# Kernel optimization log

Measured on AMD Instinct MI355X. Metric: run time of the kernel, lower is better.

## Reference

```python
import jax, jax.numpy as jnp
import numpy as np

N, C, IN_DIM, H_DIM, NUM_DEP = 16384, 4, 300, 512, 48


def setup_inputs() -> dict:
    key = jax.random.key(0)
    ks = jax.random.split(key, 12)
    # --- tree structure: 4-ary heap, reversed so children have SMALLER index than parent; root = N-1 ---
    i = np.arange(N)
    j = (N - 1) - i                                   # heap index (root j=0)
    cj = C * j[:, None] + 1 + np.arange(C)[None, :]   # heap indices of children [N,C]
    valid = cj <= N - 1
    child_idx = np.where(valid, (N - 1) - cj, 0).astype(np.int32)
    mask_h = valid.astype(np.float32)
    mask_e = valid.astype(np.float32)
    rng = np.random.default_rng(0)
    child_dep = rng.integers(0, NUM_DEP, size=(N, C)).astype(np.int32)
    leaf = ~valid.any(axis=1)
    # torch leaf branch: one virtual child with h=zeros and dep index 0
    mask_e[leaf, 0] = 1.0
    child_dep[leaf, 0] = 0
    child_idx[leaf, 0] = 0
    s = 0.02  # weight scale (stands in for xavier init)
    lin = lambda k, o, d: (jax.random.normal(k, (o, d), jnp.float32) * s)
    return {
        "x": jax.random.normal(ks[0], (N, IN_DIM), jnp.float32),
        "child_idx": jnp.asarray(child_idx),
        "child_dep": jnp.asarray(child_dep),
        "mask_h": jnp.asarray(mask_h),
        "mask_e": jnp.asarray(mask_e),
        "demb": jax.random.normal(ks[1], (NUM_DEP, H_DIM), jnp.float32) * s,
        "iux_w": lin(ks[2], 2 * H_DIM, IN_DIM), "iux_b": jnp.zeros((2 * H_DIM,), jnp.float32),
        "iuh_w": lin(ks[3], 2 * H_DIM, H_DIM), "iuh_b": jnp.zeros((2 * H_DIM,), jnp.float32),
        "iue_w": lin(ks[4], 2 * H_DIM, H_DIM), "iue_b": jnp.zeros((2 * H_DIM,), jnp.float32),
        "fx_w": lin(ks[5], H_DIM, IN_DIM), "fx_b": jnp.zeros((H_DIM,), jnp.float32),
        "fh_w": lin(ks[6], H_DIM, H_DIM), "fh_b": jnp.zeros((H_DIM,), jnp.float32),
        "fe_w": lin(ks[7], H_DIM, H_DIM), "fe_b": jnp.zeros((H_DIM,), jnp.float32),
    }


def reference(x, child_idx, child_dep, mask_h, mask_e, demb,
              iux_w, iux_b, iuh_w, iuh_b, iue_w, iue_b,
              fx_w, fx_b, fh_w, fh_b, fe_w, fe_b):
    n, h_dim = x.shape[0], fh_w.shape[0]

    def step(H, xs):
        t, xt, cidx, cdep, mh, me = xs
        ch = H[cidx] * mh[:, None]            # [C,h] child hiddens (zeros for pad / leaf virtual child)
        e = demb[cdep]                        # [C,h] dependency embeddings
        h_sum = ch.sum(0)                     # child-sum h
        e_sum = (e * me[:, None]).sum(0)      # child-sum dep embedding (leaf -> demb[0])
        iu = (xt @ iux_w.T + iux_b) + (h_sum @ iuh_w.T + iuh_b) + (e_sum @ iue_w.T + iue_b)
        i_g = jax.nn.sigmoid(iu[:h_dim])
        u = jnp.tanh(iu[h_dim:])
        f = jax.nn.sigmoid(ch @ fh_w.T + fh_b + (xt @ fx_w.T + fx_b) + e @ fe_w.T + fe_b)  # [C,h]
        h_new = jnp.tanh(i_g * u + (f * ch).sum(0))   # padded rows contribute 0 since ch=0
        return H.at[t].set(h_new), None

    H0 = jnp.zeros((n, h_dim), x.dtype)
    xs = (jnp.arange(n), x, child_idx, child_dep, mask_h, mask_e)
    Hf, _ = jax.lax.scan(step, H0, xs)
    return Hf[n - 1][None, :]   # root hidden state, shape [1, h_dim]
```

## Files before the change

kernel.cpp:

```cpp
#include <hip/hip_runtime.h>
#include <cstddef>

#define N_NODES 16384
#define HD      512
#define INDIM   300
#define INP     320
#define NDEP    48
#define NLEAF   10923
#define KT      32
#define LM      16
#define LCOL    128

typedef unsigned int u32;
typedef unsigned short u16;
typedef __attribute__((ext_vector_type(8))) short short8;
typedef __attribute__((ext_vector_type(4))) float f32x4;

typedef __attribute__((address_space(1))) const u32 as1_u32;
typedef __attribute__((address_space(3))) u32 as3_u32;

__device__ __forceinline__ float sigmoidf_(float v) {
    return 1.f / (1.f + __expf(-v));
}
__device__ __forceinline__ float tanhf_(float v) {
    v = fminf(15.f, fmaxf(-15.f, v));
    const float e = __expf(2.f * v);
    return (e - 1.f) / (e + 1.f);
}
__device__ __forceinline__ u16 f2bf(float f) {
    u32 u = __float_as_uint(f);
    u32 r = (u + 0x7fffu + ((u >> 16) & 1u)) >> 16;
    return (u16)r;
}
__device__ __forceinline__ float b2f(u16 v) {
    return __uint_as_float((u32)v << 16);
}
__device__ __forceinline__ u32 pack2(float a, float b) {
    return (u32)f2bf(a) | ((u32)f2bf(b) << 16);
}

__global__ __launch_bounds__(256)
void emb_proj_kernel(const float* __restrict__ demb,
                     const float* __restrict__ iue_w,
                     const float* __restrict__ fe_w,
                     const float* __restrict__ iux_b,
                     const float* __restrict__ iuh_b,
                     const float* __restrict__ iue_b,
                     const float* __restrict__ fx_b,
                     const float* __restrict__ fh_b,
                     const float* __restrict__ fe_b,
                     float* __restrict__ iemb,
                     float* __restrict__ femb,
                     float* __restrict__ ibc,
                     float* __restrict__ fbc)
{
    const int bo  = blockIdx.x;
    const int tid = threadIdx.x;
    if (bo == 384) {
        for (int o = tid; o < 1024; o += 256) ibc[o] = iux_b[o] + iuh_b[o] + iue_b[o];
        for (int o = tid; o < 512;  o += 256) fbc[o] = fx_b[o] + fh_b[o] + fe_b[o];
        return;
    }
    const int wave = tid >> 6;
    const int d    = tid & 63;
    const bool isI = (bo < 256);
    const int o    = (isI ? bo : bo - 256) * 4 + wave;
    const float* wrow = isI ? (iue_w + (size_t)o * HD) : (fe_w + (size_t)o * HD);
    if (d >= NDEP) return;
    const float* drow = demb + (size_t)d * HD;

    float4 a0 = make_float4(0.f, 0.f, 0.f, 0.f);
    float4 a1 = make_float4(0.f, 0.f, 0.f, 0.f);
    for (int k = 0; k < HD; k += 8) {
        const float4 wv0 = *reinterpret_cast<const float4*>(wrow + k);
        const float4 wv1 = *reinterpret_cast<const float4*>(wrow + k + 4);
        const float4 dv0 = *reinterpret_cast<const float4*>(drow + k);
        const float4 dv1 = *reinterpret_cast<const float4*>(drow + k + 4);
        a0.x = fmaf(dv0.x, wv0.x, a0.x); a0.y = fmaf(dv0.y, wv0.y, a0.y);
        a0.z = fmaf(dv0.z, wv0.z, a0.z); a0.w = fmaf(dv0.w, wv0.w, a0.w);
        a1.x = fmaf(dv1.x, wv1.x, a1.x); a1.y = fmaf(dv1.y, wv1.y, a1.y);
        a1.z = fmaf(dv1.z, wv1.z, a1.z); a1.w = fmaf(dv1.w, wv1.w, a1.w);
    }
    const float s = ((a0.x + a0.y) + (a0.z + a0.w)) + ((a1.x + a1.y) + (a1.z + a1.w));
    if (isI) iemb[(size_t)d * 1024 + o] = s;
    else     femb[(size_t)d * 512  + o] = s;
}

#define CV_T0 (N_NODES * INP)
#define CV_T1 (1536 * INP)
#define CV_T2 (1536 * HD)

__global__ __launch_bounds__(256)
void convert_all_kernel(const float* __restrict__ x,
                        const float* __restrict__ iux_w, const float* __restrict__ fx_w,
                        const float* __restrict__ iuh_w, const float* __restrict__ fh_w,
                        u16* __restrict__ xb, u16* __restrict__ WXb, u16* __restrict__ WHb)
{
    const int idx = blockIdx.x * 256 + threadIdx.x;
    if (idx < CV_T0) {
        const int r = idx / INP, k = idx - r * INP;
        xb[idx] = f2bf(k < INDIM ? x[(size_t)r * INDIM + k] : 0.f);
    } else if (idx < CV_T0 + CV_T1) {
        const int i2 = idx - CV_T0;
        const int r = i2 / INP, k = i2 - r * INP;
        float v = 0.f;
        if (k < INDIM) v = (r < 1024) ? iux_w[(size_t)r * INDIM + k]
                                      : fx_w[(size_t)(r - 1024) * INDIM + k];
        WXb[i2] = f2bf(v);
    } else {
        const int i3 = idx - CV_T0 - CV_T1;
        const int r = i3 >> 9, k = i3 & 511;
        const float v = (r < 1024) ? iuh_w[(size_t)r * HD + k]
                                   : fh_w[(size_t)(r - 1024) * HD + k];
        WHb[i3] = f2bf(v);
    }
}

__device__ __forceinline__
void gemm_body(u16* As, u16* Bs,
               const u16* __restrict__ A, int lda,
               const u16* __restrict__ B, int ldb,
               u16* __restrict__ C, int ldc,
               int M, int K, int bx, int by)
{
    const int tid  = threadIdx.x;
    const int lane = tid & 63;
    const int wave = tid >> 6;
    const int mBlk = bx * 128;
    const int nBlk = by * 128;

    const int wr = (wave >> 1) * 64;
    const int wc = (wave & 1) * 64;
    const int fr = lane & 15;
    const int kg = lane >> 4;

    f32x4 acc[4][4];
    #pragma unroll
    for (int i = 0; i < 4; ++i)
        #pragma unroll
        for (int j = 0; j < 4; ++j) acc[i][j] = (f32x4){0.f, 0.f, 0.f, 0.f};

    int offA[4], offB[4];
    #pragma unroll
    for (int it = 0; it < 4; ++it) {
        const int s   = it * 256 + tid;
        const int row = s >> 3, c = s & 7;
        const int cs  = c ^ (row & 7);
        int ga = mBlk + row; if (ga > M - 1) ga = M - 1;
        offA[it] = ga * lda + cs * 8;
        offB[it] = (nBlk + row) * ldb + cs * 8;
    }

    for (int k0 = 0; k0 < K; k0 += 64) {
        #pragma unroll
        for (int it = 0; it < 4; ++it) {
            const int ldsOff = (it * 256 + wave * 64) * 8;
            __builtin_amdgcn_global_load_lds((as1_u32*)(A + offA[it] + k0),
                                             (as3_u32*)(&As[ldsOff]), 16, 0, 0);
            __builtin_amdgcn_global_load_lds((as1_u32*)(B + offB[it] + k0),
                                             (as3_u32*)(&Bs[ldsOff]), 16, 0, 0);
        }
        __syncthreads();
        #pragma unroll
        for (int half = 0; half < 2; ++half) {
            const int ckb = half * 4 + kg;
            short8 af[4], bf[4];
            #pragma unroll
            for (int f = 0; f < 4; ++f) {
                const int ar = wr + f * 16 + fr;
                af[f] = *(const short8*)&As[ar * 64 + ((ckb ^ (ar & 7)) * 8)];
                const int br = wc + f * 16 + fr;
                bf[f] = *(const short8*)&Bs[br * 64 + ((ckb ^ (br & 7)) * 8)];
            }
            #pragma unroll
            for (int mi = 0; mi < 4; ++mi)
                #pragma unroll
                for (int ni = 0; ni < 4; ++ni)
                    acc[mi][ni] = __builtin_amdgcn_mfma_f32_16x16x32_bf16(
                                      af[mi], bf[ni], acc[mi][ni], 0, 0, 0);
        }
        __syncthreads();
    }

    #pragma unroll
    for (int mi = 0; mi < 4; ++mi) {
        const int r0 = mBlk + wr + mi * 16 + kg * 4;
        #pragma unroll
        for (int v = 0; v < 4; ++v) {
            const int r = r0 + v;
            if (r >= M) continue;
            u16* crow = C + (size_t)r * ldc + nBlk + wc + fr;
            #pragma unroll
            for (int ni = 0; ni < 4; ++ni)
                crow[ni * 16] = f2bf(acc[mi][ni][v]);
        }
    }
}

__global__ __launch_bounds__(256, 2)
void gemm_bf16_dual_kernel(const u16* __restrict__ A1, int lda1,
                           const u16* __restrict__ B1, int ldb1,
                           u16* __restrict__ C1, int ldc1, int M1, int K1,
                           int gx1, int n1,
                           const u16* __restrict__ A2, int lda2,
                           const u16* __restrict__ B2, int ldb2,
                           u16* __restrict__ C2, int ldc2, int M2, int K2,
                           int gx2)
{
    __shared__ u16 As[128 * 64];
    __shared__ u16 Bs[128 * 64];
    const int flat = blockIdx.x;
    if (flat < n1) {
        gemm_body(As, Bs, A1, lda1, B1, ldb1, C1, ldc1, M1, K1,
                  flat % gx1, flat / gx1);
    } else {
        const int f2 = flat - n1;
        gemm_body(As, Bs, A2, lda2, B2, ldb2, C2, ldc2, M2, K2,
                  f2 % gx2, f2 / gx2);
    }
}

__global__ __launch_bounds__(256)
void fused_leaf_kernel(const u16* __restrict__ XPiub,
                       const float* __restrict__ iemb, const float* __restrict__ ibc,
                       const int* __restrict__ cidx, const float* __restrict__ mh,
                       float* __restrict__ H, u16* __restrict__ Hb,
                       u16* __restrict__ HSB, int loNext)
{
    const int g   = blockIdx.x;
    const int p   = loNext + g;
    const int j2  = threadIdx.x * 2;

    int ct[4]; float cm[4];
    #pragma unroll
    for (int c = 0; c < 4; ++c) { ct[c] = cidx[p * 4 + c]; cm[c] = mh[p * 4 + c]; }

    const float2 ibci = *reinterpret_cast<const float2*>(&ibc[j2]);
    const float2 ibcu = *reinterpret_cast<const float2*>(&ibc[512 + j2]);
    const float2 iei  = *reinterpret_cast<const float2*>(&iemb[j2]);
    const float2 ieu  = *reinterpret_cast<const float2*>(&iemb[512 + j2]);

    float hs0 = 0.f, hs1 = 0.f;
    #pragma unroll
    for (int c = 0; c < 4; ++c) {
        if (cm[c] == 0.f) continue;
        const int t = ct[c];
        const u32 xi = *reinterpret_cast<const u32*>(&XPiub[(size_t)t * 1024 + j2]);
        const u32 xu = *reinterpret_cast<const u32*>(&XPiub[(size_t)t * 1024 + 512 + j2]);
        const float h0 = tanhf_(sigmoidf_(b2f((u16)xi) + iei.x + ibci.x)
                                * tanhf_(b2f((u16)xu) + ieu.x + ibcu.x));
        const float h1 = tanhf_(sigmoidf_(b2f((u16)(xi >> 16)) + iei.y + ibci.y)
                                * tanhf_(b2f((u16)(xu >> 16)) + ieu.y + ibcu.y));
        *reinterpret_cast<float2*>(&H[(size_t)t * 512 + j2]) = make_float2(h0, h1);
        *reinterpret_cast<u32*>(&Hb[(size_t)t * 512 + j2]) = pack2(h0, h1);
        hs0 += h0; hs1 += h1;
    }
    *reinterpret_cast<u32*>(&HSB[(size_t)g * 512 + j2]) = pack2(hs0, hs1);
}

__global__ __launch_bounds__(256)
void fused_combine_kernel(const u16* __restrict__ XPiub, const u16* __restrict__ XPfb,
                          const u16* __restrict__ PIUb, const u16* __restrict__ GFb,
                          const int* __restrict__ cidx, const int* __restrict__ cdep,
                          const float* __restrict__ mh, const float* __restrict__ me,
                          const float* __restrict__ iemb, const float* __restrict__ femb,
                          const float* __restrict__ ibc, const float* __restrict__ fbc,
                          float* __restrict__ H, u16* __restrict__ Hb,
                          u16* __restrict__ HSB,
                          int lo, int loNext, int isRoot, float* __restrict__ outp)
{
    const int j2 = threadIdx.x * 2;

    int ct[4]; float cm[4];
    if (isRoot) {
        ct[0] = N_NODES - 1; cm[0] = 1.f;
        ct[1] = ct[2] = ct[3] = 0; cm[1] = cm[2] = cm[3] = 0.f;
    } else {
        const int p = loNext + blockIdx.x;
        #pragma unroll
        for (int c = 0; c < 4; ++c) { ct[c] = cidx[p * 4 + c]; cm[c] = mh[p * 4 + c]; }
    }

    const float2 ibci = *reinterpret_cast<const float2*>(&ibc[j2]);
    const float2 ibcu = *reinterpret_cast<const float2*>(&ibc[512 + j2]);
    const float2 fbc2 = *reinterpret_cast<const float2*>(&fbc[j2]);

    float hs0 = 0.f, hs1 = 0.f;
    #pragma unroll
    for (int c = 0; c < 4; ++c) {
        if (cm[c] == 0.f) continue;
        const int t = ct[c];

        int ci2[4], dp2[4]; float m2[4], e2[4];
        #pragma unroll
        for (int k = 0; k < 4; ++k) {
            ci2[k] = cidx[t * 4 + k]; dp2[k] = cdep[t * 4 + k];
            m2[k]  = mh[t * 4 + k];   e2[k]  = me[t * 4 + k];
        }

        float ei0 = 0.f, ei1 = 0.f, eu0 = 0.f, eu1 = 0.f;
        #pragma unroll
        for (int k = 0; k < 4; ++k) {
            if (e2[k] != 0.f) {
                const float* ie = iemb + (size_t)dp2[k] * 1024;
                const float2 a = *reinterpret_cast<const float2*>(&ie[j2]);
                const float2 b = *reinterpret_cast<const float2*>(&ie[512 + j2]);
                ei0 = fmaf(e2[k], a.x, ei0); ei1 = fmaf(e2[k], a.y, ei1);
                eu0 = fmaf(e2[k], b.x, eu0); eu1 = fmaf(e2[k], b.y, eu1);
            }
        }

        const u32 xi = *reinterpret_cast<const u32*>(&XPiub[(size_t)t * 1024 + j2]);
        const u32 xu = *reinterpret_cast<const u32*>(&XPiub[(size_t)t * 1024 + 512 + j2]);
        const u32 pi = *reinterpret_cast<const u32*>(&PIUb[(size_t)(t - lo) * 1024 + j2]);
        const u32 pu = *reinterpret_cast<const u32*>(&PIUb[(size_t)(t - lo) * 1024 + 512 + j2]);
        const u32 xf = *reinterpret_cast<const u32*>(&XPfb[(size_t)(t - NLEAF) * 512 + j2]);

        const float iu_i0 = b2f((u16)xi) + b2f((u16)pi) + ibci.x + ei0;
        const float iu_i1 = b2f((u16)(xi >> 16)) + b2f((u16)(pi >> 16)) + ibci.y + ei1;
        const float iu_u0 = b2f((u16)xu) + b2f((u16)pu) + ibcu.x + eu0;
        const float iu_u1 = b2f((u16)(xu >> 16)) + b2f((u16)(pu >> 16)) + ibcu.y + eu1;
        const float xf0 = b2f((u16)xf) + fbc2.x;
        const float xf1 = b2f((u16)(xf >> 16)) + fbc2.y;

        float fcs0 = 0.f, fcs1 = 0.f;
        #pragma unroll
        for (int k = 0; k < 4; ++k) {
            if (m2[k] != 0.f) {
                const u32 gf = *reinterpret_cast<const u32*>(&GFb[(size_t)ci2[k] * 512 + j2]);
                const float2 fe = *reinterpret_cast<const float2*>(&femb[(size_t)dp2[k] * 512 + j2]);
                const float2 hc = *reinterpret_cast<const float2*>(&H[(size_t)ci2[k] * 512 + j2]);
                const float fv0 = b2f((u16)gf) + xf0 + fe.x;
                const float fv1 = b2f((u16)(gf >> 16)) + xf1 + fe.y;
                fcs0 = fmaf(sigmoidf_(fv0), m2[k] * hc.x, fcs0);
                fcs1 = fmaf(sigmoidf_(fv1), m2[k] * hc.y, fcs1);
            }
        }

        const float h0 = tanhf_(fmaf(sigmoidf_(iu_i0), tanhf_(iu_u0), fcs0));
        const float h1 = tanhf_(fmaf(sigmoidf_(iu_i1), tanhf_(iu_u1), fcs1));
        *reinterpret_cast<float2*>(&H[(size_t)t * 512 + j2]) = make_float2(h0, h1);
        *reinterpret_cast<u32*>(&Hb[(size_t)t * 512 + j2]) = pack2(h0, h1);
        hs0 += h0; hs1 += h1;
        if (isRoot) *reinterpret_cast<float2*>(&outp[j2]) = make_float2(h0, h1);
    }
    if (!isRoot)
        *reinterpret_cast<u32*>(&HSB[(size_t)blockIdx.x * 512 + j2]) = pack2(hs0, hs1);
}

__global__ __launch_bounds__(256)
void emb_setup_kernel(const float* __restrict__ demb,
                      const float* __restrict__ iue_w,
                      const float* __restrict__ fe_w,
                      const float* __restrict__ iux_b,
                      const float* __restrict__ iuh_b,
                      const float* __restrict__ iue_b,
                      const float* __restrict__ fx_b,
                      const float* __restrict__ fh_b,
                      const float* __restrict__ fe_b,
                      float* __restrict__ iemb,
                      float* __restrict__ femb,
                      float* __restrict__ ibc,
                      float* __restrict__ fbc)
{
    const int d   = blockIdx.x;
    const int tid = threadIdx.x;
    __shared__ float sd[HD];
    sd[tid]       = demb[d * HD + tid];
    sd[tid + 256] = demb[d * HD + 256 + tid];
    __syncthreads();

    #pragma unroll
    for (int r = 0; r < 4; ++r) {
        const int o = r * 256 + tid;
        const float* w = iue_w + (size_t)o * HD;
        float acc = 0.f;
        for (int k = 0; k < HD; k += 4) {
            const float4 wv = *reinterpret_cast<const float4*>(w + k);
            acc += sd[k] * wv.x + sd[k + 1] * wv.y + sd[k + 2] * wv.z + sd[k + 3] * wv.w;
        }
        iemb[(size_t)d * 1024 + o] = acc;
    }
    #pragma unroll
    for (int r = 0; r < 2; ++r) {
        const int o = r * 256 + tid;
        const float* w = fe_w + (size_t)o * HD;
        float acc = 0.f;
        for (int k = 0; k < HD; k += 4) {
            const float4 wv = *reinterpret_cast<const float4*>(w + k);
            acc += sd[k] * wv.x + sd[k + 1] * wv.y + sd[k + 2] * wv.z + sd[k + 3] * wv.w;
        }
        femb[(size_t)d * HD + o] = acc;
    }
    if (d == 0) {
        #pragma unroll
        for (int r = 0; r < 4; ++r) { const int o = r * 256 + tid; ibc[o] = iux_b[o] + iuh_b[o] + iue_b[o]; }
        #pragma unroll
        for (int r = 0; r < 2; ++r) { const int o = r * 256 + tid; fbc[o] = fx_b[o] + fh_b[o] + fe_b[o]; }
    }
}

__global__ __launch_bounds__(256, 2)
void level_kernel(const float* __restrict__ x,
                  const int*   __restrict__ child_idx,
                  const int*   __restrict__ child_dep,
                  const float* __restrict__ mask_h,
                  const float* __restrict__ mask_e,
                  const float* __restrict__ iux_w,
                  const float* __restrict__ iuh_w,
                  const float* __restrict__ fx_w,
                  const float* __restrict__ fh_w,
                  const float* __restrict__ iemb,
                  const float* __restrict__ femb,
                  const float* __restrict__ ibc,
                  const float* __restrict__ fbc,
                  float* __restrict__ H,
                  int tLo, int tEnd)
{
    __shared__ __align__(16) float sA[KT][68];
    __shared__ float sWI[KT][LCOL + 1];
    __shared__ float sWU[KT][LCOL + 1];
    __shared__ float sWF[KT][LCOL + 1];
    __shared__ int   sCidx[LM][4];
    __shared__ float sMh[LM][4];
    __shared__ int   sDep[LM][4];
    __shared__ float sMe[LM][4];

    const int tid  = threadIdx.x;
    const int base = tLo + blockIdx.x * LM;
    const int j0   = blockIdx.y * LCOL;

    if (tid < LM * 4) {
        const int m = tid >> 2, c = tid & 3;
        const int t = base + m;
        const bool v = (t < tEnd);
        sCidx[m][c] = v ? child_idx[t * 4 + c] : 0;
        sMh[m][c]   = v ? mask_h[t * 4 + c]    : 0.f;
        sDep[m][c]  = v ? child_dep[t * 4 + c] : 0;
        sMe[m][c]   = v ? mask_e[t * 4 + c]    : 0.f;
    }

    const int jj = tid & 63;
    const int mg = tid >> 6;

    float acc_i[4][2], acc_u[4][2], acc_fx[4][2], acc_f[4][2][4];
    #pragma unroll
    for (int mm = 0; mm < 4; ++mm)
        #pragma unroll
        for (int c2 = 0; c2 < 2; ++c2) {
            acc_i[mm][c2] = 0.f; acc_u[mm][c2] = 0.f; acc_fx[mm][c2] = 0.f;
            #pragma unroll
            for (int c = 0; c < 4; ++c) acc_f[mm][c2][c] = 0.f;
        }

    __syncthreads();

    for (int k0 = 0; k0 < HD; k0 += KT) {
        #pragma unroll
        for (int it = 0; it < 2; ++it) {
            const int chunk = tid + it * 256;
            const int mc = chunk >> 3;
            const int kk = (chunk & 7) * 4;
            const int m = mc >> 2, c = mc & 3;
            const float mhv = sMh[m][c];
            float4 v = make_float4(0.f, 0.f, 0.f, 0.f);
            if (mhv != 0.f)
                v = *reinterpret_cast<const float4*>(H + (size_t)sCidx[m][c] * HD + k0 + kk);
            sA[kk + 0][mc] = v.x; sA[kk + 1][mc] = v.y; sA[kk + 2][mc] = v.z; sA[kk + 3][mc] = v.w;
        }
        #pragma unroll
        for (int it = 0; it < 4; ++it) {
            const int chunk = tid + it * 256;
            const int row = chunk >> 3;
            const int kk = (chunk & 7) * 4;
            const float4 vI = *reinterpret_cast<const float4*>(iuh_w + (size_t)(j0 + row) * HD + k0 + kk);
            const float4 vU = *reinterpret_cast<const float4*>(iuh_w + (size_t)(j0 + row + 512) * HD + k0 + kk);
            const float4 vF = *reinterpret_cast<const float4*>(fh_w  + (size_t)(j0 + row) * HD + k0 + kk);
            sWI[kk + 0][row] = vI.x; sWI[kk + 1][row] = vI.y; sWI[kk + 2][row] = vI.z; sWI[kk + 3][row] = vI.w;
            sWU[kk + 0][row] = vU.x; sWU[kk + 1][row] = vU.y; sWU[kk + 2][row] = vU.z; sWU[kk + 3][row] = vU.w;
            sWF[kk + 0][row] = vF.x; sWF[kk + 1][row] = vF.y; sWF[kk + 2][row] = vF.z; sWF[kk + 3][row] = vF.w;
        }
        __syncthreads();
        #pragma unroll 4
        for (int k = 0; k < KT; ++k) {
            const float wi0 = sWI[k][jj], wi1 = sWI[k][jj + 64];
            const float wu0 = sWU[k][jj], wu1 = sWU[k][jj + 64];
            const float wf0 = sWF[k][jj], wf1 = sWF[k][jj + 64];
            #pragma unroll
            for (int mm = 0; mm < 4; ++mm) {
                const int m = mg + mm * 4;
                const float4 cv = *reinterpret_cast<const float4*>(&sA[k][m * 4]);
                const float hs = (cv.x + cv.y) + (cv.z + cv.w);
                acc_i[mm][0] = fmaf(hs, wi0, acc_i[mm][0]);
                acc_i[mm][1] = fmaf(hs, wi1, acc_i[mm][1]);
                acc_u[mm][0] = fmaf(hs, wu0, acc_u[mm][0]);
                acc_u[mm][1] = fmaf(hs, wu1, acc_u[mm][1]);
                acc_f[mm][0][0] = fmaf(cv.x, wf0, acc_f[mm][0][0]);
                acc_f[mm][1][0] = fmaf(cv.x, wf1, acc_f[mm][1][0]);
                acc_f[mm][0][1] = fmaf(cv.y, wf0, acc_f[mm][0][1]);
                acc_f[mm][1][1] = fmaf(cv.y, wf1, acc_f[mm][1][1]);
                acc_f[mm][0][2] = fmaf(cv.z, wf0, acc_f[mm][0][2]);
                acc_f[mm][1][2] = fmaf(cv.z, wf1, acc_f[mm][1][2]);
                acc_f[mm][0][3] = fmaf(cv.w, wf0, acc_f[mm][0][3]);
                acc_f[mm][1][3] = fmaf(cv.w, wf1, acc_f[mm][1][3]);
            }
        }
        __syncthreads();
    }

    for (int k0 = 0; k0 < INDIM; k0 += KT) {
        if (tid < 128) {
            const int m = tid >> 3;
            const int kk = (tid & 7) * 4;
            const int t = base + m;
            float4 v = make_float4(0.f, 0.f, 0.f, 0.f);
            if (t < tEnd && (k0 + kk + 3) < INDIM)
                v = *reinterpret_cast<const float4*>(x + (size_t)t * INDIM + k0 + kk);
            sA[kk + 0][m] = v.x; sA[kk + 1][m] = v.y; sA[kk + 2][m] = v.z; sA[kk + 3][m] = v.w;
        }
        #pragma unroll
        for (int it = 0; it < 4; ++it) {
            const int chunk = tid + it * 256;
            const int row = chunk >> 3;
            const int kk = (chunk & 7) * 4;
            float4 vI = make_float4(0.f, 0.f, 0.f, 0.f), vU = vI, vF = vI;
            if ((k0 + kk + 3) < INDIM) {
                vI = *reinterpret_cast<const float4*>(iux_w + (size_t)(j0 + row) * INDIM + k0 + kk);
                vU = *reinterpret_cast<const float4*>(iux_w + (size_t)(j0 + row + 512) * INDIM + k0 + kk);
                vF = *reinterpret_cast<const float4*>(fx_w  + (size_t)(j0 + row) * INDIM + k0 + kk);
            }
            sWI[kk + 0][row] = vI.x; sWI[kk + 1][row] = vI.y; sWI[kk + 2][row] = vI.z; sWI[kk + 3][row] = vI.w;
            sWU[kk + 0][row] = vU.x; sWU[kk + 1][row] = vU.y; sWU[kk + 2][row] = vU.z; sWU[kk + 3][row] = vU.w;
            sWF[kk + 0][row] = vF.x; sWF[kk + 1][row] = vF.y; sWF[kk + 2][row] = vF.z; sWF[kk + 3][row] = vF.w;
        }
        __syncthreads();
        #pragma unroll 4
        for (int k = 0; k < KT; ++k) {
            const float wi0 = sWI[k][jj], wi1 = sWI[k][jj + 64];
            const float wu0 = sWU[k][jj], wu1 = sWU[k][jj + 64];
            const float wf0 = sWF[k][jj], wf1 = sWF[k][jj + 64];
            #pragma unroll
            for (int mm = 0; mm < 4; ++mm) {
                const float xv = sA[k][mg + mm * 4];
                acc_i[mm][0]  = fmaf(xv, wi0, acc_i[mm][0]);
                acc_i[mm][1]  = fmaf(xv, wi1, acc_i[mm][1]);
                acc_u[mm][0]  = fmaf(xv, wu0, acc_u[mm][0]);
                acc_u[mm][1]  = fmaf(xv, wu1, acc_u[mm][1]);
                acc_fx[mm][0] = fmaf(xv, wf0, acc_fx[mm][0]);
                acc_fx[mm][1] = fmaf(xv, wf1, acc_fx[mm][1]);
            }
        }
        __syncthreads();
    }

    #pragma unroll
    for (int mm = 0; mm < 4; ++mm) {
        const int m = mg + mm * 4;
        const int t = base + m;
        if (t >= tEnd) continue;
        #pragma unroll
        for (int c2 = 0; c2 < 2; ++c2) {
            const int j = j0 + c2 * 64 + jj;
            float emb_i = 0.f, emb_u = 0.f;
            #pragma unroll
            for (int c = 0; c < 4; ++c) {
                const float mev = sMe[m][c];
                if (mev != 0.f) {
                    const float* ie = iemb + (size_t)sDep[m][c] * 1024;
                    emb_i = fmaf(mev, ie[j], emb_i);
                    emb_u = fmaf(mev, ie[j + 512], emb_u);
                }
            }
            const float iu_i = acc_i[mm][c2] + ibc[j] + emb_i;
            const float iu_u = acc_u[mm][c2] + ibc[j + 512] + emb_u;
            const float ig = sigmoidf_(iu_i);
            const float uu = tanhf_(iu_u);
            float fcs = 0.f;
            #pragma unroll
            for (int c = 0; c < 4; ++c) {
                const float mhv = sMh[m][c];
                if (mhv != 0.f) {
                    const float fv = acc_f[mm][c2][c] + acc_fx[mm][c2] + fbc[j]
                                   + femb[(size_t)sDep[m][c] * HD + j];
                    const float fg = sigmoidf_(fv);
                    const float chj = H[(size_t)sCidx[m][c] * HD + j] * mhv;
                    fcs = fmaf(fg, chj, fcs);
                }
            }
            H[(size_t)t * HD + j] = tanhf_(fmaf(ig, uu, fcs));
        }
    }
}

__global__ void copy_out_kernel(const float* __restrict__ H, float* __restrict__ out) {
    const int j = blockIdx.x * 256 + threadIdx.x;
    if (j < HD) out[j] = H[(size_t)(N_NODES - 1) * HD + j];
}

static const int lvlLo[8] = {0, 10923, 15019, 16043, 16299, 16363, 16379, 16383};
static const int lvlN[8]  = {10923, 4096, 1024, 256, 64, 16, 4, 1};

extern "C" void kernel_launch(void* const* d_in, const int* in_sizes, int n_in,
                              void* d_out, int out_size, void* d_ws, size_t ws_size,
                              hipStream_t stream)
{
    const float* x     = (const float*)d_in[0];
    const int*   cidx  = (const int*)  d_in[1];
    const int*   cdep  = (const int*)  d_in[2];
    const float* mh    = (const float*)d_in[3];
    const float* me    = (const float*)d_in[4];
    const float* demb  = (const float*)d_in[5];
    const float* iux_w = (const float*)d_in[6];
    const float* iux_b = (const float*)d_in[7];
    const float* iuh_w = (const float*)d_in[8];
    const float* iuh_b = (const float*)d_in[9];
    const float* iue_w = (const float*)d_in[10];
    const float* iue_b = (const float*)d_in[11];
    const float* fx_w  = (const float*)d_in[12];
    const float* fx_b  = (const float*)d_in[13];
    const float* fh_w  = (const float*)d_in[14];
    const float* fh_b  = (const float*)d_in[15];
    const float* fe_w  = (const float*)d_in[16];
    const float* fe_b  = (const float*)d_in[17];

    const size_t szH   = (size_t)N_NODES * HD * 4;
    const size_t szHb  = (size_t)N_NODES * HD * 2;
    const size_t szXPi = (size_t)N_NODES * 1024 * 2;
    const size_t szXPf = (size_t)5461 * 512 * 2;
    const size_t szGF  = (size_t)N_NODES * HD * 2;
    const size_t szPIU = (size_t)4096 * 1024 * 2;
    const size_t szHSB = (size_t)4096 * 512 * 2;
    const size_t szXB  = (size_t)N_NODES * INP * 2;
    const size_t szWX  = (size_t)1536 * INP * 2;
    const size_t szWH  = (size_t)1536 * HD * 2;
    const size_t szIE  = (size_t)NDEP * 1024 * 4;
    const size_t szFE  = (size_t)NDEP * 512 * 4;
    const size_t szIB  = 4096, szFB = 2048;
    const size_t need = szH + szHb + szXPi + szXPf + szGF + szPIU + szHSB
                      + szXB + szWX + szWH + szIE + szFE + szIB + szFB;

    if (ws_size >= need) {
        char* w = (char*)d_ws;
        float* H     = (float*)w;  w += szH;
        u16*   Hb    = (u16*)w;    w += szHb;
        u16*   XPiub = (u16*)w;    w += szXPi;
        u16*   XPfb  = (u16*)w;    w += szXPf;
        u16*   GFb   = (u16*)w;    w += szGF;
        u16*   PIUb  = (u16*)w;    w += szPIU;
        u16*   HSB   = (u16*)w;    w += szHSB;
        u16*   xb    = (u16*)w;    w += szXB;
        u16*   WXb   = (u16*)w;    w += szWX;
        u16*   WHb   = (u16*)w;    w += szWH;
        float* iemb  = (float*)w;  w += szIE;
        float* femb  = (float*)w;  w += szFE;
        float* ibc   = (float*)w;  w += szIB;
        float* fbc   = (float*)w;  w += szFB;

        {
            const int tot = CV_T0 + CV_T1 + CV_T2;
            hipLaunchKernelGGL(convert_all_kernel, dim3((tot + 255) / 256), dim3(256), 0, stream,
                               x, iux_w, fx_w, iuh_w, fh_w, xb, WXb, WHb);
        }
        hipLaunchKernelGGL(emb_proj_kernel, dim3(385), dim3(256), 0, stream,
                           demb, iue_w, fe_w, iux_b, iuh_b, iue_b, fx_b, fh_b, fe_b,
                           iemb, femb, ibc, fbc);

        {
            const int gx1 = N_NODES / 128, n1 = gx1 * (1024 / 128);
            const int gx2 = (5461 + 127) / 128;
            const int n2  = gx2 * (512 / 128);
            hipLaunchKernelGGL(gemm_bf16_dual_kernel, dim3(n1 + n2), dim3(256), 0, stream,
                               xb, INP, WXb, INP, XPiub, 1024, N_NODES, INP, gx1, n1,
                               xb + (size_t)NLEAF * INP, INP, WXb + (size_t)1024 * INP, INP,
                               XPfb, 512, 5461, INP, gx2);
        }

        hipLaunchKernelGGL(fused_leaf_kernel, dim3(lvlN[1]), dim3(256), 0, stream,
                           XPiub, iemb, ibc, cidx, mh, H, Hb, HSB, lvlLo[1]);

        for (int l = 1; l < 8; ++l) {
            const int pLo = lvlLo[l - 1], pN = lvlN[l - 1];
            const int lo  = lvlLo[l],     n  = lvlN[l];
            const int gx1 = (pN + 127) / 128, n1 = gx1 * (512 / 128);
            const int gx2 = (n + 127) / 128,  n2 = gx2 * (1024 / 128);
            hipLaunchKernelGGL(gemm_bf16_dual_kernel, dim3(n1 + n2), dim3(256), 0, stream,
                               Hb + (size_t)pLo * HD, HD, WHb + (size_t)1024 * HD, HD,
                               GFb + (size_t)pLo * HD, HD, pN, HD, gx1, n1,
                               HSB, HD, WHb, HD, PIUb, 1024, n, HD, gx2);
            const int isRoot = (l == 7);
            const int gridC  = isRoot ? 1 : lvlN[l + 1];
            const int loNext = isRoot ? 0 : lvlLo[l + 1];
            hipLaunchKernelGGL(fused_combine_kernel, dim3(gridC), dim3(256), 0, stream,
                               XPiub, XPfb, PIUb, GFb, cidx, cdep, mh, me,
                               iemb, femb, ibc, fbc, H, Hb, HSB,
                               lo, loNext, isRoot, (float*)d_out);
        }
        return;
    }

    float* ws   = (float*)d_ws;
    float* H    = ws;
    float* iemb = H + (size_t)N_NODES * HD;
    float* femb = iemb + (size_t)NDEP * 1024;
    float* ibc  = femb + (size_t)NDEP * HD;
    float* fbc  = ibc + 1024;

    hipLaunchKernelGGL(emb_setup_kernel, dim3(NDEP), dim3(256), 0, stream,
                       demb, iue_w, fe_w, iux_b, iuh_b, iue_b, fx_b, fh_b, fe_b,
                       iemb, femb, ibc, fbc);
    for (int l = 0; l < 8; ++l) {
        dim3 grid((lvlN[l] + LM - 1) / LM, HD / LCOL);
        hipLaunchKernelGGL(level_kernel, grid, dim3(256), 0, stream,
                           x, cidx, cdep, mh, me, iux_w, iuh_w, fx_w, fh_w,
                           iemb, femb, ibc, fbc, H, lvlLo[l], lvlLo[l] + lvlN[l]);
    }
    hipLaunchKernelGGL(copy_out_kernel, dim3(2), dim3(256), 0, stream, H, (float*)d_out);
}
```

Before: 248.6 us.

## Fuse all stages into one persistent kernel with software grid barriers

Replaces the sequence of about 18 kernel launches (convert, embedding projection, input GEMM, leaf, and per-level GEMM/combine pairs) with a single persistent kernel of 512 blocks. The blocks loop over each former grid and sync between stages with an atomic-counter grid barrier, plus a tiny kernel that zeroes the counters. The aim is to remove launch and inter-kernel gap overhead, which dominates the small upper tree levels. The risks are barrier spin cost, deadlock if 512 blocks cannot all be co-resident, and loss of per-stage occupancy tuning.

```diff
diff --git a/kernel.cpp b/kernel.cpp
--- a/kernel.cpp
+++ b/kernel.cpp
@@ -7,6 +7,8 @@
 #define INP     320
 #define NDEP    48
 #define NLEAF   10923
+#define NINT    5461
+#define NBLK    512
 #define KT      32
 #define LM      16
 #define LCOL    128
@@ -19,6 +21,9 @@
 typedef __attribute__((address_space(1))) const u32 as1_u32;
 typedef __attribute__((address_space(3))) u32 as3_u32;
 
+__device__ const int d_lvlLo[9] = {0, 10923, 15019, 16043, 16299, 16363, 16379, 16383, 16384};
+__device__ const int d_lvlN[8]  = {10923, 4096, 1024, 256, 64, 16, 4, 1};
+
 __device__ __forceinline__ float sigmoidf_(float v) {
     return 1.f / (1.f + __expf(-v));
 }
@@ -39,81 +44,21 @@
     return (u32)f2bf(a) | ((u32)f2bf(b) << 16);
 }
 
-__global__ __launch_bounds__(256)
-void emb_proj_kernel(const float* __restrict__ demb,
-                     const float* __restrict__ iue_w,
-                     const float* __restrict__ fe_w,
-                     const float* __restrict__ iux_b,
-                     const float* __restrict__ iuh_b,
-                     const float* __restrict__ iue_b,
-                     const float* __restrict__ fx_b,
-                     const float* __restrict__ fh_b,
-                     const float* __restrict__ fe_b,
-                     float* __restrict__ iemb,
-                     float* __restrict__ femb,
-                     float* __restrict__ ibc,
-                     float* __restrict__ fbc)
-{
-    const int bo  = blockIdx.x;
-    const int tid = threadIdx.x;
-    if (bo == 384) {
-        for (int o = tid; o < 1024; o += 256) ibc[o] = iux_b[o] + iuh_b[o] + iue_b[o];
-        for (int o = tid; o < 512;  o += 256) fbc[o] = fx_b[o] + fh_b[o] + fe_b[o];
-        return;
-    }
-    const int wave = tid >> 6;
-    const int d    = tid & 63;
-    const bool isI = (bo < 256);
-    const int o    = (isI ? bo : bo - 256) * 4 + wave;
-    const float* wrow = isI ? (iue_w + (size_t)o * HD) : (fe_w + (size_t)o * HD);
-    if (d >= NDEP) return;
-    const float* drow = demb + (size_t)d * HD;
-
-    float4 a0 = make_float4(0.f, 0.f, 0.f, 0.f);
-    float4 a1 = make_float4(0.f, 0.f, 0.f, 0.f);
-    for (int k = 0; k < HD; k += 8) {
-        const float4 wv0 = *reinterpret_cast<const float4*>(wrow + k);
-        const float4 wv1 = *reinterpret_cast<const float4*>(wrow + k + 4);
-        const float4 dv0 = *reinterpret_cast<const float4*>(drow + k);
-        const float4 dv1 = *reinterpret_cast<const float4*>(drow + k + 4);
-        a0.x = fmaf(dv0.x, wv0.x, a0.x); a0.y = fmaf(dv0.y, wv0.y, a0.y);
-        a0.z = fmaf(dv0.z, wv0.z, a0.z); a0.w = fmaf(dv0.w, wv0.w, a0.w);
-        a1.x = fmaf(dv1.x, wv1.x, a1.x); a1.y = fmaf(dv1.y, wv1.y, a1.y);
-        a1.z = fmaf(dv1.z, wv1.z, a1.z); a1.w = fmaf(dv1.w, wv1.w, a1.w);
-    }
-    const float s = ((a0.x + a0.y) + (a0.z + a0.w)) + ((a1.x + a1.y) + (a1.z + a1.w));
-    if (isI) iemb[(size_t)d * 1024 + o] = s;
-    else     femb[(size_t)d * 512  + o] = s;
-}
-
-#define CV_T0 (N_NODES * INP)
-#define CV_T1 (1536 * INP)
-#define CV_T2 (1536 * HD)
-
-__global__ __launch_bounds__(256)
-void convert_all_kernel(const float* __restrict__ x,
-                        const float* __restrict__ iux_w, const float* __restrict__ fx_w,
-                        const float* __restrict__ iuh_w, const float* __restrict__ fh_w,
-                        u16* __restrict__ xb, u16* __restrict__ WXb, u16* __restrict__ WHb)
-{
-    const int idx = blockIdx.x * 256 + threadIdx.x;
-    if (idx < CV_T0) {
-        const int r = idx / INP, k = idx - r * INP;
-        xb[idx] = f2bf(k < INDIM ? x[(size_t)r * INDIM + k] : 0.f);
-    } else if (idx < CV_T0 + CV_T1) {
-        const int i2 = idx - CV_T0;
-        const int r = i2 / INP, k = i2 - r * INP;
-        float v = 0.f;
-        if (k < INDIM) v = (r < 1024) ? iux_w[(size_t)r * INDIM + k]
-                                      : fx_w[(size_t)(r - 1024) * INDIM + k];
-        WXb[i2] = f2bf(v);
-    } else {
-        const int i3 = idx - CV_T0 - CV_T1;
-        const int r = i3 >> 9, k = i3 & 511;
-        const float v = (r < 1024) ? iuh_w[(size_t)r * HD + k]
-                                   : fh_w[(size_t)(r - 1024) * HD + k];
-        WHb[i3] = f2bf(v);
-    }
+__device__ __forceinline__ void gridbar(u32* cnt, int idx) {
+    __syncthreads();
+    if (threadIdx.x == 0) {
+        __threadfence();
+        __hip_atomic_fetch_add(&cnt[idx * 16], 1u, __ATOMIC_ACQ_REL, __HIP_MEMORY_SCOPE_AGENT);
+        while (__hip_atomic_load(&cnt[idx * 16], __ATOMIC_RELAXED, __HIP_MEMORY_SCOPE_AGENT) < (u32)NBLK)
+            __builtin_amdgcn_s_sleep(2);
+        __threadfence();
+    }
+    __syncthreads();
+}
+
+__global__ void init_cnt_kernel(u32* cnt) {
+    const int i = threadIdx.x;
+    cnt[i] = 0; cnt[i + 256] = 0;
 }
 
 __device__ __forceinline__
@@ -197,39 +142,15 @@
     }
 }
 
-__global__ __launch_bounds__(256, 2)
-void gemm_bf16_dual_kernel(const u16* __restrict__ A1, int lda1,
-                           const u16* __restrict__ B1, int ldb1,
-                           u16* __restrict__ C1, int ldc1, int M1, int K1,
-                           int gx1, int n1,
-                           const u16* __restrict__ A2, int lda2,
-                           const u16* __restrict__ B2, int ldb2,
-                           u16* __restrict__ C2, int ldc2, int M2, int K2,
-                           int gx2)
+__device__ __forceinline__
+void dev_leaf(int g, const u16* __restrict__ XPiub,
+              const float* __restrict__ iemb, const float* __restrict__ ibc,
+              const int* __restrict__ cidx, const float* __restrict__ mh,
+              float* __restrict__ H, u16* __restrict__ Hb,
+              u16* __restrict__ HSB, int loNext)
 {
-    __shared__ u16 As[128 * 64];
-    __shared__ u16 Bs[128 * 64];
-    const int flat = blockIdx.x;
-    if (flat < n1) {
-        gemm_body(As, Bs, A1, lda1, B1, ldb1, C1, ldc1, M1, K1,
-                  flat % gx1, flat / gx1);
-    } else {
-        const int f2 = flat - n1;
-        gemm_body(As, Bs, A2, lda2, B2, ldb2, C2, ldc2, M2, K2,
-                  f2 % gx2, f2 / gx2);
-    }
-}
-
-__global__ __launch_bounds__(256)
-void fused_leaf_kernel(const u16* __restrict__ XPiub,
-                       const float* __restrict__ iemb, const float* __restrict__ ibc,
-                       const int* __restrict__ cidx, const float* __restrict__ mh,
-                       float* __restrict__ H, u16* __restrict__ Hb,
-                       u16* __restrict__ HSB, int loNext)
-{
-    const int g   = blockIdx.x;
-    const int p   = loNext + g;
-    const int j2  = threadIdx.x * 2;
+    const int p  = loNext + g;
+    const int j2 = threadIdx.x * 2;
 
     int ct[4]; float cm[4];
     #pragma unroll
@@ -258,16 +179,15 @@
     *reinterpret_cast<u32*>(&HSB[(size_t)g * 512 + j2]) = pack2(hs0, hs1);
 }
 
-__global__ __launch_bounds__(256)
-void fused_combine_kernel(const u16* __restrict__ XPiub, const u16* __restrict__ XPfb,
-                          const u16* __restrict__ PIUb, const u16* __restrict__ GFb,
-                          const int* __restrict__ cidx, const int* __restrict__ cdep,
-                          const float* __restrict__ mh, const float* __restrict__ me,
-                          const float* __restrict__ iemb, const float* __restrict__ femb,
-                          const float* __restrict__ ibc, const float* __restrict__ fbc,
-                          float* __restrict__ H, u16* __restrict__ Hb,
-                          u16* __restrict__ HSB,
-                          int lo, int loNext, int isRoot, float* __restrict__ outp)
+__device__ __forceinline__
+void dev_combine(int g, const u16* __restrict__ XPiub, const u16* __restrict__ XPfb,
+                 const u16* __restrict__ PIUb, const u16* __restrict__ GFb,
+                 const int* __restrict__ cidx, const int* __restrict__ cdep,
+                 const float* __restrict__ mh, const float* __restrict__ me,
+                 const float* __restrict__ iemb, const float* __restrict__ femb,
+                 const float* __restrict__ ibc, const float* __restrict__ fbc,
+                 float* __restrict__ H, u16* __restrict__ Hb, u16* __restrict__ HSB,
+                 int lo, int loNext, int isRoot, float* __restrict__ outp)
 {
     const int j2 = threadIdx.x * 2;
 
@@ -276,7 +196,7 @@
         ct[0] = N_NODES - 1; cm[0] = 1.f;
         ct[1] = ct[2] = ct[3] = 0; cm[1] = cm[2] = cm[3] = 0.f;
     } else {
-        const int p = loNext + blockIdx.x;
+        const int p = loNext + g;
         #pragma unroll
         for (int c = 0; c < 4; ++c) { ct[c] = cidx[p * 4 + c]; cm[c] = mh[p * 4 + c]; }
     }
@@ -345,7 +265,138 @@
         if (isRoot) *reinterpret_cast<float2*>(&outp[j2]) = make_float2(h0, h1);
     }
     if (!isRoot)
-        *reinterpret_cast<u32*>(&HSB[(size_t)blockIdx.x * 512 + j2]) = pack2(hs0, hs1);
+        *reinterpret_cast<u32*>(&HSB[(size_t)g * 512 + j2]) = pack2(hs0, hs1);
+}
+
+#define CV_T0 (N_NODES * INP)
+#define CV_T1 (1536 * INP)
+#define CV_T2 (1536 * HD)
+#define CV_TOT (CV_T0 + CV_T1 + CV_T2)
+
+__global__ __launch_bounds__(256, 2)
+void mega_kernel(const float* __restrict__ x,
+                 const int* __restrict__ cidx, const int* __restrict__ cdep,
+                 const float* __restrict__ mh, const float* __restrict__ me,
+                 const float* __restrict__ demb,
+                 const float* __restrict__ iux_w, const float* __restrict__ iux_b,
+                 const float* __restrict__ iuh_w, const float* __restrict__ iuh_b,
+                 const float* __restrict__ iue_w, const float* __restrict__ iue_b,
+                 const float* __restrict__ fx_w, const float* __restrict__ fx_b,
+                 const float* __restrict__ fh_w, const float* __restrict__ fh_b,
+                 const float* __restrict__ fe_w, const float* __restrict__ fe_b,
+                 float* __restrict__ H, u16* __restrict__ Hb,
+                 u16* __restrict__ XPiub, u16* __restrict__ XPfb,
+                 u16* __restrict__ GFb, u16* __restrict__ PIUb,
+                 u16* __restrict__ HSB, u16* __restrict__ xb,
+                 u16* __restrict__ WXb, u16* __restrict__ WHb,
+                 float* __restrict__ iemb, float* __restrict__ femb,
+                 float* __restrict__ ibc, float* __restrict__ fbc,
+                 u32* __restrict__ cnt, float* __restrict__ outp)
+{
+    __shared__ u16 As[128 * 64];
+    __shared__ u16 Bs[128 * 64];
+    const int tid = threadIdx.x;
+    const int bid = blockIdx.x;
+    int b = 0;
+
+    for (int idx = bid * 256 + tid; idx < CV_TOT; idx += NBLK * 256) {
+        if (idx < CV_T0) {
+            const int r = idx / INP, k = idx - r * INP;
+            xb[idx] = f2bf(k < INDIM ? x[(size_t)r * INDIM + k] : 0.f);
+        } else if (idx < CV_T0 + CV_T1) {
+            const int i2 = idx - CV_T0;
+            const int r = i2 / INP, k = i2 - r * INP;
+            float v = 0.f;
+            if (k < INDIM) v = (r < 1024) ? iux_w[(size_t)r * INDIM + k]
+                                          : fx_w[(size_t)(r - 1024) * INDIM + k];
+            WXb[i2] = f2bf(v);
+        } else {
+            const int i3 = idx - CV_T0 - CV_T1;
+            const int r = i3 >> 9, k = i3 & 511;
+            const float v = (r < 1024) ? iuh_w[(size_t)r * HD + k]
+                                       : fh_w[(size_t)(r - 1024) * HD + k];
+            WHb[i3] = f2bf(v);
+        }
+    }
+    for (int bo = bid; bo < 385; bo += NBLK) {
+        if (bo == 384) {
+            for (int o = tid; o < 1024; o += 256) ibc[o] = iux_b[o] + iuh_b[o] + iue_b[o];
+            for (int o = tid; o < 512;  o += 256) fbc[o] = fx_b[o] + fh_b[o] + fe_b[o];
+        } else {
+            const int wave = tid >> 6;
+            const int d    = tid & 63;
+            const bool isI = (bo < 256);
+            const int o    = (isI ? bo : bo - 256) * 4 + wave;
+            if (d < NDEP) {
+                const float* wrow = isI ? (iue_w + (size_t)o * HD) : (fe_w + (size_t)o * HD);
+                const float* drow = demb + (size_t)d * HD;
+                float4 a0 = make_float4(0.f, 0.f, 0.f, 0.f);
+                float4 a1 = make_float4(0.f, 0.f, 0.f, 0.f);
+                for (int k = 0; k < HD; k += 8) {
+                    const float4 wv0 = *reinterpret_cast<const float4*>(wrow + k);
+                    const float4 wv1 = *reinterpret_cast<const float4*>(wrow + k + 4);
+                    const float4 dv0 = *reinterpret_cast<const float4*>(drow + k);
+                    const float4 dv1 = *reinterpret_cast<const float4*>(drow + k + 4);
+                    a0.x = fmaf(dv0.x, wv0.x, a0.x); a0.y = fmaf(dv0.y, wv0.y, a0.y);
+                    a0.z = fmaf(dv0.z, wv0.z, a0.z); a0.w = fmaf(dv0.w, wv0.w, a0.w);
+                    a1.x = fmaf(dv1.x, wv1.x, a1.x); a1.y = fmaf(dv1.y, wv1.y, a1.y);
+                    a1.z = fmaf(dv1.z, wv1.z, a1.z); a1.w = fmaf(dv1.w, wv1.w, a1.w);
+                }
+                const float s = ((a0.x + a0.y) + (a0.z + a0.w)) + ((a1.x + a1.y) + (a1.z + a1.w));
+                if (isI) iemb[(size_t)d * 1024 + o] = s;
+                else     femb[(size_t)d * 512  + o] = s;
+            }
+        }
+    }
+    gridbar(cnt, b++);
+
+    {
+        const int gx1 = N_NODES / 128, n1 = gx1 * (1024 / 128);
+        const int gx2 = (NINT + 127) / 128;
+        const int n2  = gx2 * (512 / 128);
+        for (int j = bid; j < n1 + n2; j += NBLK) {
+            if (j < n1)
+                gemm_body(As, Bs, xb, INP, WXb, INP, XPiub, 1024, N_NODES, INP,
+                          j % gx1, j / gx1);
+            else {
+                const int f2 = j - n1;
+                gemm_body(As, Bs, xb + (size_t)NLEAF * INP, INP,
+                          WXb + (size_t)1024 * INP, INP, XPfb, 512, NINT, INP,
+                          f2 % gx2, f2 / gx2);
+            }
+        }
+    }
+    gridbar(cnt, b++);
+
+    for (int g = bid; g < 4096; g += NBLK)
+        dev_leaf(g, XPiub, iemb, ibc, cidx, mh, H, Hb, HSB, d_lvlLo[1]);
+    gridbar(cnt, b++);
+
+    for (int l = 1; l < 8; ++l) {
+        const int pLo = d_lvlLo[l - 1], pN = d_lvlN[l - 1];
+        const int lo  = d_lvlLo[l],     n  = d_lvlN[l];
+        const int gx1 = (pN + 127) / 128, n1 = gx1 * (512 / 128);
+        const int gx2 = (n + 127) / 128,  n2 = gx2 * (1024 / 128);
+        for (int j = bid; j < n1 + n2; j += NBLK) {
+            if (j < n1)
+                gemm_body(As, Bs, Hb + (size_t)pLo * HD, HD, WHb + (size_t)1024 * HD, HD,
+                          GFb + (size_t)pLo * HD, HD, pN, HD, j % gx1, j / gx1);
+            else {
+                const int f2 = j - n1;
+                gemm_body(As, Bs, HSB, HD, WHb, HD, PIUb, 1024, n, HD,
+                          f2 % gx2, f2 / gx2);
+            }
+        }
+        gridbar(cnt, b++);
+
+        const int isRoot = (l == 7);
+        const int gridC  = isRoot ? 1 : d_lvlN[l + 1];
+        const int loNext = isRoot ? 0 : d_lvlLo[l + 1];
+        for (int g = bid; g < gridC; g += NBLK)
+            dev_combine(g, XPiub, XPfb, PIUb, GFb, cidx, cdep, mh, me,
+                        iemb, femb, ibc, fbc, H, Hb, HSB, lo, loNext, isRoot, outp);
+        if (l < 7) gridbar(cnt, b++);
+    }
 }
 
 __global__ __launch_bounds__(256)
@@ -626,7 +677,7 @@
     const size_t szH   = (size_t)N_NODES * HD * 4;
     const size_t szHb  = (size_t)N_NODES * HD * 2;
     const size_t szXPi = (size_t)N_NODES * 1024 * 2;
-    const size_t szXPf = (size_t)5461 * 512 * 2;
+    const size_t szXPf = (size_t)NINT * 512 * 2;
     const size_t szGF  = (size_t)N_NODES * HD * 2;
     const size_t szPIU = (size_t)4096 * 1024 * 2;
     const size_t szHSB = (size_t)4096 * 512 * 2;
@@ -635,9 +686,9 @@
     const size_t szWH  = (size_t)1536 * HD * 2;
     const size_t szIE  = (size_t)NDEP * 1024 * 4;
     const size_t szFE  = (size_t)NDEP * 512 * 4;
-    const size_t szIB  = 4096, szFB = 2048;
+    const size_t szIB  = 4096, szFB = 2048, szCNT = 2048;
     const size_t need = szH + szHb + szXPi + szXPf + szGF + szPIU + szHSB
-                      + szXB + szWX + szWH + szIE + szFE + szIB + szFB;
+                      + szXB + szWX + szWH + szIE + szFE + szIB + szFB + szCNT;
 
     if (ws_size >= need) {
         char* w = (char*)d_ws;
@@ -655,46 +706,15 @@
         float* femb  = (float*)w;  w += szFE;
         float* ibc   = (float*)w;  w += szIB;
         float* fbc   = (float*)w;  w += szFB;
-
-        {
-            const int tot = CV_T0 + CV_T1 + CV_T2;
-            hipLaunchKernelGGL(convert_all_kernel, dim3((tot + 255) / 256), dim3(256), 0, stream,
-                               x, iux_w, fx_w, iuh_w, fh_w, xb, WXb, WHb);
-        }
-        hipLaunchKernelGGL(emb_proj_kernel, dim3(385), dim3(256), 0, stream,
-                           demb, iue_w, fe_w, iux_b, iuh_b, iue_b, fx_b, fh_b, fe_b,
-                           iemb, femb, ibc, fbc);
-
-        {
-            const int gx1 = N_NODES / 128, n1 = gx1 * (1024 / 128);
-            const int gx2 = (5461 + 127) / 128;
-            const int n2  = gx2 * (512 / 128);
-            hipLaunchKernelGGL(gemm_bf16_dual_kernel, dim3(n1 + n2), dim3(256), 0, stream,
-                               xb, INP, WXb, INP, XPiub, 1024, N_NODES, INP, gx1, n1,
-                               xb + (size_t)NLEAF * INP, INP, WXb + (size_t)1024 * INP, INP,
-                               XPfb, 512, 5461, INP, gx2);
-        }
-
-        hipLaunchKernelGGL(fused_leaf_kernel, dim3(lvlN[1]), dim3(256), 0, stream,
-                           XPiub, iemb, ibc, cidx, mh, H, Hb, HSB, lvlLo[1]);
-
-        for (int l = 1; l < 8; ++l) {
-            const int pLo = lvlLo[l - 1], pN = lvlN[l - 1];
-            const int lo  = lvlLo[l],     n  = lvlN[l];
-            const int gx1 = (pN + 127) / 128, n1 = gx1 * (512 / 128);
-            const int gx2 = (n + 127) / 128,  n2 = gx2 * (1024 / 128);
-            hipLaunchKernelGGL(gemm_bf16_dual_kernel, dim3(n1 + n2), dim3(256), 0, stream,
-                               Hb + (size_t)pLo * HD, HD, WHb + (size_t)1024 * HD, HD,
-                               GFb + (size_t)pLo * HD, HD, pN, HD, gx1, n1,
-                               HSB, HD, WHb, HD, PIUb, 1024, n, HD, gx2);
-            const int isRoot = (l == 7);
-            const int gridC  = isRoot ? 1 : lvlN[l + 1];
-            const int loNext = isRoot ? 0 : lvlLo[l + 1];
-            hipLaunchKernelGGL(fused_combine_kernel, dim3(gridC), dim3(256), 0, stream,
-                               XPiub, XPfb, PIUb, GFb, cidx, cdep, mh, me,
-                               iemb, femb, ibc, fbc, H, Hb, HSB,
-                               lo, loNext, isRoot, (float*)d_out);
-        }
+        u32*   cnt   = (u32*)w;    w += szCNT;
+
+        hipLaunchKernelGGL(init_cnt_kernel, dim3(1), dim3(256), 0, stream, cnt);
+        hipLaunchKernelGGL(mega_kernel, dim3(NBLK), dim3(256), 0, stream,
+                           x, cidx, cdep, mh, me, demb,
+                           iux_w, iux_b, iuh_w, iuh_b, iue_w, iue_b,
+                           fx_w, fx_b, fh_w, fh_b, fe_w, fe_b,
+                           H, Hb, XPiub, XPfb, GFb, PIUb, HSB, xb, WXb, WHb,
+                           iemb, femb, ibc, fbc, cnt, (float*)d_out);
         return;
     }
 
```

Result: slower. 987.8 us (+297.4%).
